# Kernel tuning notes

Hardware: AMD Instinct MI355X
Metric: run time of the kernel (lower is better)

Reference implementation:

```python
import jax, jax.numpy as jnp
import numpy as np

EMBED_DIM = 768
NUM_HEADS = 12
D_K = EMBED_DIM // NUM_HEADS


def setup_inputs() -> dict:
    key = jax.random.key(0)
    k_x, k_qkv, k_out_w, k_out_b = jax.random.split(key, 4)
    B, S = 1, 4096
    x = jax.random.normal(k_x, (B, S, EMBED_DIM), dtype=jnp.float32)
    # nn.Linear(embed_dim, 3*embed_dim, bias=False): weight [3E, E], y = x @ W^T
    scale_qkv = 1.0 / np.sqrt(EMBED_DIM)
    w_qkv = jax.random.uniform(k_qkv, (3 * EMBED_DIM, EMBED_DIM), dtype=jnp.float32,
                               minval=-scale_qkv, maxval=scale_qkv)
    w_out = jax.random.uniform(k_out_w, (EMBED_DIM, EMBED_DIM), dtype=jnp.float32,
                               minval=-scale_qkv, maxval=scale_qkv)
    b_out = jax.random.uniform(k_out_b, (EMBED_DIM,), dtype=jnp.float32,
                               minval=-scale_qkv, maxval=scale_qkv)
    return {"x": x, "w_qkv": w_qkv, "w_out": w_out, "b_out": b_out}


def reference(x, w_qkv, w_out, b_out):
    B, S, E = x.shape
    H, Dk = NUM_HEADS, D_K
    # qkv projection: [B,S,3E] -> [3,B,H,S,Dk]
    qkv = jnp.einsum('bse,fe->bsf', x, w_qkv)
    qkv = qkv.reshape(B, S, 3, H, Dk).transpose(2, 0, 3, 1, 4)
    q, k, v = qkv[0], qkv[1], qkv[2]
    # scaled dot-product attention, full [B,H,S,S] scores (naive, faithful)
    scores = jnp.einsum('bhsd,bhtd->bhst', q, k) / jnp.sqrt(jnp.float32(Dk))
    attn = jax.nn.softmax(scores, axis=-1)
    # dropout is identity in eval/deterministic baseline
    out = jnp.einsum('bhst,bhtd->bhsd', attn, v)
    out = out.transpose(0, 2, 1, 3).reshape(B, S, E)
    return jnp.einsum('bse,fe->bsf', out, w_out) + b_out
```

## Files before the change

### kernel.cpp

```cpp
#include <hip/hip_runtime.h>
#include <hip/hip_bf16.h>

constexpr int S_LEN   = 4096;
constexpr int EMB     = 768;
constexpr int NH      = 12;
constexpr int DK      = 64;
constexpr int QKV_DIM = 3 * EMB;
constexpr int NSPLIT  = 2;
constexpr int TSPLIT  = S_LEN / NSPLIT;

typedef short bf16x8 __attribute__((ext_vector_type(8)));
typedef float f32x4  __attribute__((ext_vector_type(4)));
typedef unsigned short u16;

__device__ inline u16 f2bf(float x) {
  unsigned u = __float_as_uint(x);
  unsigned r = u + 0x7fffu + ((u >> 16) & 1u);
  return (u16)(r >> 16);
}
__device__ inline float bf2f(u16 h) {
  return __uint_as_float(((unsigned)h) << 16);
}

__device__ inline void gld16(unsigned* lds, const unsigned* g) {
  __builtin_amdgcn_global_load_lds(
      (const __attribute__((address_space(1))) unsigned*)g,
      (__attribute__((address_space(3))) unsigned*)lds, 16, 0, 0);
}

#define LOG2E 1.4426950408889634f

__global__ __launch_bounds__(256) void cast_bf16(
    const float* __restrict__ src, u16* __restrict__ dst, int n8)
{
  for (int i = blockIdx.x * 256 + threadIdx.x; i < n8; i += gridDim.x * 256) {
    float4 a = reinterpret_cast<const float4*>(src)[2 * i + 0];
    float4 b = reinterpret_cast<const float4*>(src)[2 * i + 1];
    ushort4 h0, h1;
    const float* ap = reinterpret_cast<const float*>(&a);
    const float* bp = reinterpret_cast<const float*>(&b);
#pragma unroll
    for (int j = 0; j < 4; ++j) {
      reinterpret_cast<u16*>(&h0)[j] = f2bf(ap[j]);
      reinterpret_cast<u16*>(&h1)[j] = f2bf(bp[j]);
    }
    reinterpret_cast<ushort4*>(dst)[2 * i + 0] = h0;
    reinterpret_cast<ushort4*>(dst)[2 * i + 1] = h1;
  }
}

template<int MODE>
__global__ __launch_bounds__(256) void gemm_bf16_nt(
    const u16* __restrict__ A, const u16* __restrict__ B,
    const float* __restrict__ bias,
    u16* __restrict__ Cb, float* __restrict__ Cf,
    int M, int N, int K)
{
  __shared__ __align__(16) u16 sA[128 * 64];
  __shared__ __align__(16) u16 sB[128 * 64];

  const int tid  = threadIdx.x;
  const int w    = tid >> 6;
  const int l    = tid & 63;
  const int lg   = l >> 4;
  const int lr   = l & 15;
  const int wr   = w >> 1;
  const int wc   = w & 1;
  const int brow = blockIdx.x * 128;
  const int bcol = blockIdx.y * 128;

  const int srow = l >> 3;
  const int sslot = l & 7;

  f32x4 acc[4][4] = {};

  for (int k0 = 0; k0 < K; k0 += 64) {
#pragma unroll
    for (int cc = 0; cc < 4; ++cc) {
      int c = w * 4 + cc;
      int row = c * 8 + srow;
      int kswz = (sslot ^ (row & 7)) * 8;
      size_t aoff = (size_t)(brow + row) * K + k0 + kswz;
      size_t boff = (size_t)(bcol + row) * K + k0 + kswz;
      gld16((unsigned*)(sA + c * 512), (const unsigned*)(A + aoff));
      gld16((unsigned*)(sB + c * 512), (const unsigned*)(B + boff));
    }
    __syncthreads();

#pragma unroll
    for (int ks = 0; ks < 2; ++ks) {
      bf16x8 fa[4], fb[4];
#pragma unroll
      for (int i = 0; i < 4; ++i) {
        int arow = wr * 64 + i * 16 + lr;
        int brow_ = wc * 64 + i * 16 + lr;
        fa[i] = *reinterpret_cast<const bf16x8*>(
            &sA[arow * 64 + (((lg + 4 * ks) ^ (arow & 7)) << 3)]);
        fb[i] = *reinterpret_cast<const bf16x8*>(
            &sB[brow_ * 64 + (((lg + 4 * ks) ^ (brow_ & 7)) << 3)]);
      }
#pragma unroll
      for (int mi = 0; mi < 4; ++mi)
#pragma unroll
        for (int ni = 0; ni < 4; ++ni)
          acc[mi][ni] = __builtin_amdgcn_mfma_f32_16x16x32_bf16(
              fa[mi], fb[ni], acc[mi][ni], 0, 0, 0);
    }
    __syncthreads();
  }

  if (MODE == 0) {
    const float qscale = (bcol < EMB) ? 0.125f * LOG2E : 1.0f;
#pragma unroll
    for (int mi = 0; mi < 4; ++mi)
#pragma unroll
      for (int ni = 0; ni < 4; ++ni)
#pragma unroll
        for (int r = 0; r < 4; ++r) {
          size_t m = brow + wr * 64 + mi * 16 + 4 * lg + r;
          size_t n = bcol + wc * 64 + ni * 16 + lr;
          Cb[m * N + n] = f2bf(acc[mi][ni][r] * qscale);
        }
  } else {
#pragma unroll
    for (int mi = 0; mi < 4; ++mi)
#pragma unroll
      for (int ni = 0; ni < 4; ++ni)
#pragma unroll
        for (int r = 0; r < 4; ++r) {
          size_t m = brow + wr * 64 + mi * 16 + 4 * lg + r;
          size_t n = bcol + wc * 64 + ni * 16 + lr;
          Cf[m * N + n] = acc[mi][ni][r] + bias[n];
        }
  }
}

__device__ inline int key7(int row) { return (row ^ (row >> 3)) & 7; }
__device__ inline int swz16(int row, int s) {
  return row * 64 + ((s ^ key7(row)) << 3);
}
__device__ inline int swz32(int row, int p) {
  return row * 32 + ((((p >> 2) ^ key7(row)) << 2) | (p & 3));
}

__global__ __launch_bounds__(256, 3) void flash_split(
    const u16* __restrict__ qkv, float* __restrict__ Sp,
    float* __restrict__ lp)
{
  __shared__ __align__(16) u16 Ks[2][64 * 64];
  __shared__ __align__(16) u16 Vt[2][64 * 64];
  __shared__ __align__(16) u16 Ps[4][32 * 64];

  const int tid = threadIdx.x;
  const int w   = tid >> 6;
  const int l   = tid & 63;
  const int lg  = l >> 4;
  const int lr  = l & 15;

  const int bid   = blockIdx.x;
  const int sbid  = (bid & 7) * 96 + (bid >> 3);
  const int split = sbid & 1;
  const int qb    = ((sbid >> 1) & 31) * 128;
  const int h     = sbid >> 6;
  const int tbeg  = split * TSPLIT;

  unsigned* Pw = (unsigned*)Ps[w];

  const int tq  = tid >> 3;
  const int vgs = tid & 7;

  int kfO[4][2], vfO[4][2], paO[2][2], pwO[2][4], vcO[8];
#pragma unroll
  for (int tt = 0; tt < 4; ++tt)
#pragma unroll
    for (int ks = 0; ks < 2; ++ks) {
      kfO[tt][ks] = swz16(tt * 16 + lr, 4 * ks + lg);
      vfO[tt][ks] = kfO[tt][ks];
    }
#pragma unroll
  for (int qf = 0; qf < 2; ++qf) {
#pragma unroll
    for (int ks = 0; ks < 2; ++ks)
      paO[qf][ks] = swz16(qf * 16 + lr, 4 * ks + lg);
#pragma unroll
    for (int tt = 0; tt < 4; ++tt)
      pwO[qf][tt] = swz32(qf * 16 + lr, 8 * tt + 2 * lg);
  }
#pragma unroll
  for (int j = 0; j < 8; ++j)
    vcO[j] = swz32(vgs * 8 + j, tq);

  const int kt0 = tid >> 3, kg0 = tid & 7;
  const int kgo0 = kt0 * QKV_DIM + ((kg0 ^ key7(kt0)) << 3);
  const int kgo1 = (kt0 + 32) * QKV_DIM + ((kg0 ^ key7(kt0 + 32)) << 3);

  const u16* kg = qkv + EMB + h * DK + (size_t)tbeg * QKV_DIM;
  const u16* vg = qkv + 2 * EMB + h * DK +
                  ((size_t)tbeg + 2 * tq) * QKV_DIM + vgs * 8;

  bf16x8 qfr[2][2];
#pragma unroll
  for (int qf = 0; qf < 2; ++qf)
#pragma unroll
    for (int ks = 0; ks < 2; ++ks)
      qfr[qf][ks] = *reinterpret_cast<const bf16x8*>(
          qkv + (size_t)(qb + w * 32 + qf * 16 + lr) * QKV_DIM + h * DK + ks * 32 + lg * 8);

  bf16x8 ones;
#pragma unroll
  for (int i = 0; i < 8; ++i) ones[i] = (short)0x3F80;

  f32x4 acc[2][4] = {};
  f32x4 lacc[2]   = {};
  uint4 vr0, vr1;

  gld16((unsigned*)(Ks[0] + tid * 8),        (const unsigned*)(kg + kgo0));
  gld16((unsigned*)(Ks[0] + 2048 + tid * 8), (const unsigned*)(kg + kgo1));
  vr0 = *reinterpret_cast<const uint4*>(vg);
  vr1 = *reinterpret_cast<const uint4*>(vg + QKV_DIM);

  constexpr int NT = TSPLIT / 64;

#define FL_ITER(CUR, IT)                                                       \
  {                                                                            \
                              \
    {                                                                          \
      unsigned* vdst = (unsigned*)Vt[CUR];                                     \
      const unsigned* a0 = reinterpret_cast<const unsigned*>(&vr0);            \
      const unsigned* a1 = reinterpret_cast<const unsigned*>(&vr1);            \
      _Pragma("unroll")                                                        \
      for (int j = 0; j < 8; ++j) {                                            \
        unsigned sel = (j & 1) ? 0x07060302u : 0x05040100u;                    \
        vdst[vcO[j]] = __builtin_amdgcn_perm(a1[j >> 1], a0[j >> 1], sel);     \
      }                                                                        \
    }                                                                          \
    __syncthreads();                                                           \
                                         \
    if ((IT) + 1 < NT) {                                                       \
      kg += 64 * QKV_DIM;                                                      \
      vg += 64 * QKV_DIM;                                                      \
      gld16((unsigned*)(Ks[(CUR) ^ 1] + tid * 8),                              \
            (const unsigned*)(kg + kgo0));                                     \
      gld16((unsigned*)(Ks[(CUR) ^ 1] + 2048 + tid * 8),                       \
            (const unsigned*)(kg + kgo1));                                     \
      vr0 = *reinterpret_cast<const uint4*>(vg);                               \
      vr1 = *reinterpret_cast<const uint4*>(vg + QKV_DIM);                     \
    }                                                                          \
                                              \
    {                                                                          \
      bf16x8 kf[4][2];                                                         \
      _Pragma("unroll")                                                        \
      for (int tt = 0; tt < 4; ++tt) {                                         \
        kf[tt][0] = *reinterpret_cast<const bf16x8*>(&Ks[CUR][kfO[tt][0]]);    \
        kf[tt][1] = *reinterpret_cast<const bf16x8*>(&Ks[CUR][kfO[tt][1]]);    \
      }                                                                        \
      _Pragma("unroll")                                                        \
      for (int qf = 0; qf < 2; ++qf) {                                         \
        f32x4 s[4] = {};                                                       \
        __builtin_amdgcn_s_setprio(1);                                         \
        _Pragma("unroll")                                                      \
        for (int tt = 0; tt < 4; ++tt) {                                       \
          s[tt] = __builtin_amdgcn_mfma_f32_16x16x32_bf16(                     \
              kf[tt][0], qfr[qf][0], s[tt], 0, 0, 0);                          \
          s[tt] = __builtin_amdgcn_mfma_f32_16x16x32_bf16(                     \
              kf[tt][1], qfr[qf][1], s[tt], 0, 0, 0);                          \
        }                                                                      \
        __builtin_amdgcn_s_setprio(0);                                         \
        _Pragma("unroll")                                                      \
        for (int tt = 0; tt < 4; ++tt) {                                       \
          float p0 = exp2f(s[tt][0]);                                          \
          float p1 = exp2f(s[tt][1]);                                          \
          float p2 = exp2f(s[tt][2]);                                          \
          float p3 = exp2f(s[tt][3]);                                          \
          uint2 pv;                                                            \
          pv.x = __builtin_amdgcn_perm(__float_as_uint(p1),                    \
                                       __float_as_uint(p0), 0x07060302u);      \
          pv.y = __builtin_amdgcn_perm(__float_as_uint(p3),                    \
                                       __float_as_uint(p2), 0x07060302u);      \
          *reinterpret_cast<uint2*>(&Pw[pwO[qf][tt]]) = pv;                    \
        }                                                                      \
      }                                                                        \
      __builtin_amdgcn_s_setprio(1);                                           \
      _Pragma("unroll")                                                        \
      for (int ks = 0; ks < 2; ++ks) {                                         \
        bf16x8 pa[2];                                                          \
        pa[0] = *reinterpret_cast<const bf16x8*>(&Ps[w][paO[0][ks]]);          \
        pa[1] = *reinterpret_cast<const bf16x8*>(&Ps[w][paO[1][ks]]);          \
        lacc[0] = __builtin_amdgcn_mfma_f32_16x16x32_bf16(                     \
            ones, pa[0], lacc[0], 0, 0, 0);                                    \
        lacc[1] = __builtin_amdgcn_mfma_f32_16x16x32_bf16(                     \
            ones, pa[1], lacc[1], 0, 0, 0);                                    \
        _Pragma("unroll")                                                      \
        for (int dt = 0; dt < 4; ++dt) {                                       \
          bf16x8 vf = *reinterpret_cast<const bf16x8*>(&Vt[CUR][vfO[dt][ks]]); \
          acc[0][dt] = __builtin_amdgcn_mfma_f32_16x16x32_bf16(                \
              vf, pa[0], acc[0][dt], 0, 0, 0);                                 \
          acc[1][dt] = __builtin_amdgcn_mfma_f32_16x16x32_bf16(                \
              vf, pa[1], acc[1][dt], 0, 0, 0);                                 \
        }                                                                      \
      }                                                                        \
      __builtin_amdgcn_s_setprio(0);                                           \
    }                                                                          \
  }

  for (int it = 0; it < NT; it += 2) {
    FL_ITER(0, it);
    FL_ITER(1, it + 1);
  }
#undef FL_ITER

#pragma unroll
  for (int qf = 0; qf < 2; ++qf) {
    int q = qb + w * 32 + qf * 16 + lr;
    size_t base = ((size_t)split * S_LEN + q) * EMB + h * DK;
#pragma unroll
    for (int dt = 0; dt < 4; ++dt)
      *reinterpret_cast<float4*>(&Sp[base + dt * 16 + 4 * lg]) =
          *reinterpret_cast<float4*>(&acc[qf][dt]);
    if (lg == 0)
      lp[((size_t)split * NH + h) * S_LEN + q] = lacc[qf][0];
  }
}

__global__ __launch_bounds__(256) void combine_splits(
    const float* __restrict__ Sp, const float* __restrict__ lp,
    u16* __restrict__ ao)
{
  constexpr int N4 = S_LEN * EMB / 4;
  for (int i = blockIdx.x * 256 + threadIdx.x; i < N4; i += gridDim.x * 256) {
    int q = i / 192;
    int t = i - q * 192;
    int h = t >> 4;
    float la = lp[(size_t)h * S_LEN + q];
    float lb = lp[(size_t)(NH + h) * S_LEN + q];
    float inv = 1.0f / (la + lb);
    float4 s0 = reinterpret_cast<const float4*>(Sp)[i];
    float4 s1 = reinterpret_cast<const float4*>(Sp)[N4 + i];
    ushort4 o;
    o.x = f2bf((s0.x + s1.x) * inv);
    o.y = f2bf((s0.y + s1.y) * inv);
    o.z = f2bf((s0.z + s1.z) * inv);
    o.w = f2bf((s0.w + s1.w) * inv);
    reinterpret_cast<ushort4*>(ao)[i] = o;
  }
}

extern "C" void kernel_launch(void* const* d_in, const int* in_sizes, int n_in,
                              void* d_out, int out_size, void* d_ws, size_t ws_size,
                              hipStream_t stream) {
  const float* x     = (const float*)d_in[0];
  const float* w_qkv = (const float*)d_in[1];
  const float* w_out = (const float*)d_in[2];
  const float* b_out = (const float*)d_in[3];
  float* out = (float*)d_out;

  constexpr size_t NX  = (size_t)S_LEN * EMB;
  constexpr size_t NWQ = (size_t)QKV_DIM * EMB;
  constexpr size_t NWO = (size_t)EMB * EMB;
  constexpr size_t NQ  = (size_t)S_LEN * QKV_DIM;

  u16* xb    = (u16*)d_ws;
  u16* wqb   = xb + NX;
  u16* wob   = wqb + NWQ;
  u16* qkvb  = wob + NWO;
  float* Sp  = (float*)(qkvb + NQ);
  float* lp  = Sp + (size_t)NSPLIT * S_LEN * EMB;
  u16* aob   = xb;

  dim3 blk(256);

  cast_bf16<<<dim3(512), blk, 0, stream>>>(x,     xb,  (int)(NX / 8));
  cast_bf16<<<dim3(256), blk, 0, stream>>>(w_qkv, wqb, (int)(NWQ / 8));
  cast_bf16<<<dim3(128), blk, 0, stream>>>(w_out, wob, (int)(NWO / 8));

  gemm_bf16_nt<0><<<dim3(S_LEN / 128, QKV_DIM / 128), blk, 0, stream>>>(
      xb, wqb, nullptr, qkvb, nullptr, S_LEN, QKV_DIM, EMB);

  flash_split<<<dim3(768), blk, 0, stream>>>(qkvb, Sp, lp);
  combine_splits<<<dim3(1024), blk, 0, stream>>>(Sp, lp, aob);

  gemm_bf16_nt<1><<<dim3(S_LEN / 128, EMB / 128), blk, 0, stream>>>(
      aob, wob, b_out, nullptr, out, S_LEN, EMB, EMB);
}
```

Before: 144.2 us.

## Enlarge flash query tile to 256, split keys four ways, fuse cast kernels

```diff
diff --git a/kernel.cpp b/kernel.cpp
--- a/kernel.cpp
+++ b/kernel.cpp
@@ -6,7 +6,7 @@
 constexpr int NH      = 12;
 constexpr int DK      = 64;
 constexpr int QKV_DIM = 3 * EMB;
-constexpr int NSPLIT  = 2;
+constexpr int NSPLIT  = 4;
 constexpr int TSPLIT  = S_LEN / NSPLIT;
 
 typedef short bf16x8 __attribute__((ext_vector_type(8)));
@@ -28,12 +28,28 @@
       (__attribute__((address_space(3))) unsigned*)lds, 16, 0, 0);
 }
 
+__device__ inline float fast_exp2(float x) {
+#if __has_builtin(__builtin_amdgcn_exp2f)
+  return __builtin_amdgcn_exp2f(x);
+#else
+  float r;
+  asm("v_exp_f32 %0, %1" : "=v"(r) : "v"(x));
+  return r;
+#endif
+}
+
 #define LOG2E 1.4426950408889634f
 
-__global__ __launch_bounds__(256) void cast_bf16(
-    const float* __restrict__ src, u16* __restrict__ dst, int n8)
+__global__ __launch_bounds__(256) void cast_bf16_fused(
+    const float* __restrict__ s0, u16* __restrict__ d0, int n0,
+    const float* __restrict__ s1, u16* __restrict__ d1, int n1,
+    const float* __restrict__ s2, u16* __restrict__ d2, int n2)
 {
-  for (int i = blockIdx.x * 256 + threadIdx.x; i < n8; i += gridDim.x * 256) {
+  const float* src; u16* dst; int n8, b0, nb;
+  if (blockIdx.x < 512)      { src = s0; dst = d0; n8 = n0; b0 = 0;   nb = 512; }
+  else if (blockIdx.x < 768) { src = s1; dst = d1; n8 = n1; b0 = 512; nb = 256; }
+  else                       { src = s2; dst = d2; n8 = n2; b0 = 768; nb = 128; }
+  for (int i = (blockIdx.x - b0) * 256 + threadIdx.x; i < n8; i += nb * 256) {
     float4 a = reinterpret_cast<const float4*>(src)[2 * i + 0];
     float4 b = reinterpret_cast<const float4*>(src)[2 * i + 1];
     ushort4 h0, h1;
@@ -159,8 +175,8 @@
 
   const int bid   = blockIdx.x;
   const int sbid  = (bid & 7) * 96 + (bid >> 3);
-  const int split = sbid & 1;
-  const int qb    = ((sbid >> 1) & 31) * 128;
+  const int split = sbid & 3;
+  const int qb    = ((sbid >> 2) & 15) * 256;
   const int h     = sbid >> 6;
   const int tbeg  = split * TSPLIT;
 
@@ -169,22 +185,20 @@
   const int tq  = tid >> 3;
   const int vgs = tid & 7;
 
-  int kfO[4][2], vfO[4][2], paO[2][2], pwO[2][4], vcO[8];
+  int kfO[4][2], paO[2][2], pwO[2][4], vcO[8];
 #pragma unroll
   for (int tt = 0; tt < 4; ++tt)
 #pragma unroll
-    for (int ks = 0; ks < 2; ++ks) {
+    for (int ks = 0; ks < 2; ++ks)
       kfO[tt][ks] = swz16(tt * 16 + lr, 4 * ks + lg);
-      vfO[tt][ks] = kfO[tt][ks];
-    }
-#pragma unroll
-  for (int qf = 0; qf < 2; ++qf) {
+#pragma unroll
+  for (int hq = 0; hq < 2; ++hq) {
 #pragma unroll
     for (int ks = 0; ks < 2; ++ks)
-      paO[qf][ks] = swz16(qf * 16 + lr, 4 * ks + lg);
+      paO[hq][ks] = swz16(hq * 16 + lr, 4 * ks + lg);
 #pragma unroll
     for (int tt = 0; tt < 4; ++tt)
-      pwO[qf][tt] = swz32(qf * 16 + lr, 8 * tt + 2 * lg);
+      pwO[hq][tt] = swz32(hq * 16 + lr, 8 * tt + 2 * lg);
   }
 #pragma unroll
   for (int j = 0; j < 8; ++j)
@@ -198,20 +212,20 @@
   const u16* vg = qkv + 2 * EMB + h * DK +
                   ((size_t)tbeg + 2 * tq) * QKV_DIM + vgs * 8;
 
-  bf16x8 qfr[2][2];
-#pragma unroll
-  for (int qf = 0; qf < 2; ++qf)
+  bf16x8 qfr[4][2];
+#pragma unroll
+  for (int qf = 0; qf < 4; ++qf)
 #pragma unroll
     for (int ks = 0; ks < 2; ++ks)
       qfr[qf][ks] = *reinterpret_cast<const bf16x8*>(
-          qkv + (size_t)(qb + w * 32 + qf * 16 + lr) * QKV_DIM + h * DK + ks * 32 + lg * 8);
+          qkv + (size_t)(qb + w * 64 + qf * 16 + lr) * QKV_DIM + h * DK + ks * 32 + lg * 8);
 
   bf16x8 ones;
 #pragma unroll
   for (int i = 0; i < 8; ++i) ones[i] = (short)0x3F80;
 
-  f32x4 acc[2][4] = {};
-  f32x4 lacc[2]   = {};
+  f32x4 acc[4][4] = {};
+  f32x4 lacc[4]   = {};
   uint4 vr0, vr1;
 
   gld16((unsigned*)(Ks[0] + tid * 8),        (const unsigned*)(kg + kgo0));
@@ -220,6 +234,56 @@
   vr1 = *reinterpret_cast<const uint4*>(vg + QKV_DIM);
 
   constexpr int NT = TSPLIT / 64;
+
+#define QKT_PACK(QF)                                                           \
+  {                                                                            \
+    f32x4 s[4] = {};                                                           \
+    __builtin_amdgcn_s_setprio(1);                                             \
+    _Pragma("unroll")                                                          \
+    for (int tt = 0; tt < 4; ++tt) {                                           \
+      s[tt] = __builtin_amdgcn_mfma_f32_16x16x32_bf16(                         \
+          kf[tt][0], qfr[QF][0], s[tt], 0, 0, 0);                              \
+      s[tt] = __builtin_amdgcn_mfma_f32_16x16x32_bf16(                         \
+          kf[tt][1], qfr[QF][1], s[tt], 0, 0, 0);                              \
+    }                                                                          \
+    __builtin_amdgcn_s_setprio(0);                                             \
+    _Pragma("unroll")                                                          \
+    for (int tt = 0; tt < 4; ++tt) {                                           \
+      float p0 = fast_exp2(s[tt][0]);                                          \
+      float p1 = fast_exp2(s[tt][1]);                                          \
+      float p2 = fast_exp2(s[tt][2]);                                          \
+      float p3 = fast_exp2(s[tt][3]);                                          \
+      uint2 pv;                                                                \
+      pv.x = __builtin_amdgcn_perm(__float_as_uint(p1),                        \
+                                   __float_as_uint(p0), 0x07060302u);          \
+      pv.y = __builtin_amdgcn_perm(__float_as_uint(p3),                        \
+                                   __float_as_uint(p2), 0x07060302u);          \
+      *reinterpret_cast<uint2*>(&Pw[pwO[(QF) & 1][tt]]) = pv;                  \
+    }                                                                          \
+  }
+
+#define PV_HALF(HF, CUR)                                                       \
+  {                                                                            \
+    __builtin_amdgcn_s_setprio(1);                                             \
+    _Pragma("unroll")                                                          \
+    for (int ks = 0; ks < 2; ++ks) {                                           \
+      bf16x8 pa0 = *reinterpret_cast<const bf16x8*>(&Ps[w][paO[0][ks]]);       \
+      bf16x8 pa1 = *reinterpret_cast<const bf16x8*>(&Ps[w][paO[1][ks]]);       \
+      lacc[2 * (HF) + 0] = __builtin_amdgcn_mfma_f32_16x16x32_bf16(            \
+          ones, pa0, lacc[2 * (HF) + 0], 0, 0, 0);                             \
+      lacc[2 * (HF) + 1] = __builtin_amdgcn_mfma_f32_16x16x32_bf16(            \
+          ones, pa1, lacc[2 * (HF) + 1], 0, 0, 0);                             \
+      _Pragma("unroll")                                                        \
+      for (int dt = 0; dt < 4; ++dt) {                                         \
+        bf16x8 vf = *reinterpret_cast<const bf16x8*>(&Vt[CUR][kfO[dt][ks]]);   \
+        acc[2 * (HF) + 0][dt] = __builtin_amdgcn_mfma_f32_16x16x32_bf16(       \
+            vf, pa0, acc[2 * (HF) + 0][dt], 0, 0, 0);                          \
+        acc[2 * (HF) + 1][dt] = __builtin_amdgcn_mfma_f32_16x16x32_bf16(       \
+            vf, pa1, acc[2 * (HF) + 1][dt], 0, 0, 0);                          \
+      }                                                                        \
+    }                                                                          \
+    __builtin_amdgcn_s_setprio(0);                                             \
+  }
 
 #define FL_ITER(CUR, IT)                                                       \
   {                                                                            \
@@ -246,7 +310,7 @@
       vr0 = *reinterpret_cast<const uint4*>(vg);                               \
       vr1 = *reinterpret_cast<const uint4*>(vg + QKV_DIM);                     \
     }                                                                          \
-                                              \
+                   \
     {                                                                          \
       bf16x8 kf[4][2];                                                         \
       _Pragma("unroll")                                                        \
@@ -254,52 +318,12 @@
         kf[tt][0] = *reinterpret_cast<const bf16x8*>(&Ks[CUR][kfO[tt][0]]);    \
         kf[tt][1] = *reinterpret_cast<const bf16x8*>(&Ks[CUR][kfO[tt][1]]);    \
       }                                                                        \
-      _Pragma("unroll")                                                        \
-      for (int qf = 0; qf < 2; ++qf) {                                         \
-        f32x4 s[4] = {};                                                       \
-        __builtin_amdgcn_s_setprio(1);                                         \
-        _Pragma("unroll")                                                      \
-        for (int tt = 0; tt < 4; ++tt) {                                       \
-          s[tt] = __builtin_amdgcn_mfma_f32_16x16x32_bf16(                     \
-              kf[tt][0], qfr[qf][0], s[tt], 0, 0, 0);                          \
-          s[tt] = __builtin_amdgcn_mfma_f32_16x16x32_bf16(                     \
-              kf[tt][1], qfr[qf][1], s[tt], 0, 0, 0);                          \
-        }                                                                      \
-        __builtin_amdgcn_s_setprio(0);                                         \
-        _Pragma("unroll")                                                      \
-        for (int tt = 0; tt < 4; ++tt) {                                       \
-          float p0 = exp2f(s[tt][0]);                                          \
-          float p1 = exp2f(s[tt][1]);                                          \
-          float p2 = exp2f(s[tt][2]);                                          \
-          float p3 = exp2f(s[tt][3]);                                          \
-          uint2 pv;                                                            \
-          pv.x = __builtin_amdgcn_perm(__float_as_uint(p1),                    \
-                                       __float_as_uint(p0), 0x07060302u);      \
-          pv.y = __builtin_amdgcn_perm(__float_as_uint(p3),                    \
-                                       __float_as_uint(p2), 0x07060302u);      \
-          *reinterpret_cast<uint2*>(&Pw[pwO[qf][tt]]) = pv;                    \
-        }                                                                      \
-      }                                                                        \
-      __builtin_amdgcn_s_setprio(1);                                           \
-      _Pragma("unroll")                                                        \
-      for (int ks = 0; ks < 2; ++ks) {                                         \
-        bf16x8 pa[2];                                                          \
-        pa[0] = *reinterpret_cast<const bf16x8*>(&Ps[w][paO[0][ks]]);          \
-        pa[1] = *reinterpret_cast<const bf16x8*>(&Ps[w][paO[1][ks]]);          \
-        lacc[0] = __builtin_amdgcn_mfma_f32_16x16x32_bf16(                     \
-            ones, pa[0], lacc[0], 0, 0, 0);                                    \
-        lacc[1] = __builtin_amdgcn_mfma_f32_16x16x32_bf16(                     \
-            ones, pa[1], lacc[1], 0, 0, 0);                                    \
-        _Pragma("unroll")                                                      \
-        for (int dt = 0; dt < 4; ++dt) {                                       \
-          bf16x8 vf = *reinterpret_cast<const bf16x8*>(&Vt[CUR][vfO[dt][ks]]); \
-          acc[0][dt] = __builtin_amdgcn_mfma_f32_16x16x32_bf16(                \
-              vf, pa[0], acc[0][dt], 0, 0, 0);                                 \
-          acc[1][dt] = __builtin_amdgcn_mfma_f32_16x16x32_bf16(                \
-              vf, pa[1], acc[1][dt], 0, 0, 0);                                 \
-        }                                                                      \
-      }                                                                        \
-      __builtin_amdgcn_s_setprio(0);                                           \
+      QKT_PACK(0);                                                             \
+      QKT_PACK(1);                                                             \
+      PV_HALF(0, CUR);                                                         \
+      QKT_PACK(2);                                                             \
+      QKT_PACK(3);                                                             \
+      PV_HALF(1, CUR);                                                         \
     }                                                                          \
   }
 
@@ -308,10 +332,12 @@
     FL_ITER(1, it + 1);
   }
 #undef FL_ITER
-
-#pragma unroll
-  for (int qf = 0; qf < 2; ++qf) {
-    int q = qb + w * 32 + qf * 16 + lr;
+#undef PV_HALF
+#undef QKT_PACK
+
+#pragma unroll
+  for (int qf = 0; qf < 4; ++qf) {
+    int q = qb + w * 64 + qf * 16 + lr;
     size_t base = ((size_t)split * S_LEN + q) * EMB + h * DK;
 #pragma unroll
     for (int dt = 0; dt < 4; ++dt)
@@ -331,16 +357,20 @@
     int q = i / 192;
     int t = i - q * 192;
     int h = t >> 4;
-    float la = lp[(size_t)h * S_LEN + q];
-    float lb = lp[(size_t)(NH + h) * S_LEN + q];
-    float inv = 1.0f / (la + lb);
+    float lsum = 0.0f;
+#pragma unroll
+    for (int s = 0; s < NSPLIT; ++s)
+      lsum += lp[((size_t)s * NH + h) * S_LEN + q];
+    float inv = 1.0f / lsum;
     float4 s0 = reinterpret_cast<const float4*>(Sp)[i];
     float4 s1 = reinterpret_cast<const float4*>(Sp)[N4 + i];
+    float4 s2 = reinterpret_cast<const float4*>(Sp)[2 * N4 + i];
+    float4 s3 = reinterpret_cast<const float4*>(Sp)[3 * N4 + i];
     ushort4 o;
-    o.x = f2bf((s0.x + s1.x) * inv);
-    o.y = f2bf((s0.y + s1.y) * inv);
-    o.z = f2bf((s0.z + s1.z) * inv);
-    o.w = f2bf((s0.w + s1.w) * inv);
+    o.x = f2bf((s0.x + s1.x + s2.x + s3.x) * inv);
+    o.y = f2bf((s0.y + s1.y + s2.y + s3.y) * inv);
+    o.z = f2bf((s0.z + s1.z + s2.z + s3.z) * inv);
+    o.w = f2bf((s0.w + s1.w + s2.w + s3.w) * inv);
     reinterpret_cast<ushort4*>(ao)[i] = o;
   }
 }
@@ -369,9 +399,8 @@
 
   dim3 blk(256);
 
-  cast_bf16<<<dim3(512), blk, 0, stream>>>(x,     xb,  (int)(NX / 8));
-  cast_bf16<<<dim3(256), blk, 0, stream>>>(w_qkv, wqb, (int)(NWQ / 8));
-  cast_bf16<<<dim3(128), blk, 0, stream>>>(w_out, wob, (int)(NWO / 8));
+  cast_bf16_fused<<<dim3(896), blk, 0, stream>>>(
+      x, xb, (int)(NX / 8), w_qkv, wqb, (int)(NWQ / 8), w_out, wob, (int)(NWO / 8));
 
   gemm_bf16_nt<0><<<dim3(S_LEN / 128, QKV_DIM / 128), blk, 0, stream>>>(
       xb, wqb, nullptr, qkvb, nullptr, S_LEN, QKV_DIM, EMB);
```

After: 338.2 us. 2.35x slower.

## Use four KV splits with 256-row Q tiles, fast exp2, fused casts

Applied to the files above, without the earlier changes.

```diff
diff --git a/kernel.cpp b/kernel.cpp
--- a/kernel.cpp
+++ b/kernel.cpp
@@ -6,7 +6,7 @@
 constexpr int NH      = 12;
 constexpr int DK      = 64;
 constexpr int QKV_DIM = 3 * EMB;
-constexpr int NSPLIT  = 2;
+constexpr int NSPLIT  = 4;
 constexpr int TSPLIT  = S_LEN / NSPLIT;
 
 typedef short bf16x8 __attribute__((ext_vector_type(8)));
@@ -28,12 +28,28 @@
       (__attribute__((address_space(3))) unsigned*)lds, 16, 0, 0);
 }
 
+__device__ inline float fast_exp2(float x) {
+#if __has_builtin(__builtin_amdgcn_exp2f)
+  return __builtin_amdgcn_exp2f(x);
+#else
+  float r;
+  asm("v_exp_f32 %0, %1" : "=v"(r) : "v"(x));
+  return r;
+#endif
+}
+
 #define LOG2E 1.4426950408889634f
 
-__global__ __launch_bounds__(256) void cast_bf16(
-    const float* __restrict__ src, u16* __restrict__ dst, int n8)
+__global__ __launch_bounds__(256) void cast_bf16_fused(
+    const float* __restrict__ s0, u16* __restrict__ d0, int n0,
+    const float* __restrict__ s1, u16* __restrict__ d1, int n1,
+    const float* __restrict__ s2, u16* __restrict__ d2, int n2)
 {
-  for (int i = blockIdx.x * 256 + threadIdx.x; i < n8; i += gridDim.x * 256) {
+  const float* src; u16* dst; int n8, b0, nb;
+  if (blockIdx.x < 512)      { src = s0; dst = d0; n8 = n0; b0 = 0;   nb = 512; }
+  else if (blockIdx.x < 768) { src = s1; dst = d1; n8 = n1; b0 = 512; nb = 256; }
+  else                       { src = s2; dst = d2; n8 = n2; b0 = 768; nb = 128; }
+  for (int i = (blockIdx.x - b0) * 256 + threadIdx.x; i < n8; i += nb * 256) {
     float4 a = reinterpret_cast<const float4*>(src)[2 * i + 0];
     float4 b = reinterpret_cast<const float4*>(src)[2 * i + 1];
     ushort4 h0, h1;
@@ -143,13 +159,13 @@
   return row * 32 + ((((p >> 2) ^ key7(row)) << 2) | (p & 3));
 }
 
-__global__ __launch_bounds__(256, 3) void flash_split(
+__global__ __launch_bounds__(256) void flash_split(
     const u16* __restrict__ qkv, float* __restrict__ Sp,
     float* __restrict__ lp)
 {
   __shared__ __align__(16) u16 Ks[2][64 * 64];
   __shared__ __align__(16) u16 Vt[2][64 * 64];
-  __shared__ __align__(16) u16 Ps[4][32 * 64];
+  __shared__ __align__(16) u16 Ps[4][64 * 64];
 
   const int tid = threadIdx.x;
   const int w   = tid >> 6;
@@ -159,8 +175,8 @@
 
   const int bid   = blockIdx.x;
   const int sbid  = (bid & 7) * 96 + (bid >> 3);
-  const int split = sbid & 1;
-  const int qb    = ((sbid >> 1) & 31) * 128;
+  const int split = sbid & 3;
+  const int qb    = ((sbid >> 2) & 15) * 256;
   const int h     = sbid >> 6;
   const int tbeg  = split * TSPLIT;
 
@@ -169,16 +185,14 @@
   const int tq  = tid >> 3;
   const int vgs = tid & 7;
 
-  int kfO[4][2], vfO[4][2], paO[2][2], pwO[2][4], vcO[8];
+  int kfO[4][2], paO[4][2], pwO[4][4], vcO[8];
 #pragma unroll
   for (int tt = 0; tt < 4; ++tt)
 #pragma unroll
-    for (int ks = 0; ks < 2; ++ks) {
+    for (int ks = 0; ks < 2; ++ks)
       kfO[tt][ks] = swz16(tt * 16 + lr, 4 * ks + lg);
-      vfO[tt][ks] = kfO[tt][ks];
-    }
-#pragma unroll
-  for (int qf = 0; qf < 2; ++qf) {
+#pragma unroll
+  for (int qf = 0; qf < 4; ++qf) {
 #pragma unroll
     for (int ks = 0; ks < 2; ++ks)
       paO[qf][ks] = swz16(qf * 16 + lr, 4 * ks + lg);
@@ -198,20 +212,20 @@
   const u16* vg = qkv + 2 * EMB + h * DK +
                   ((size_t)tbeg + 2 * tq) * QKV_DIM + vgs * 8;
 
-  bf16x8 qfr[2][2];
-#pragma unroll
-  for (int qf = 0; qf < 2; ++qf)
+  bf16x8 qfr[4][2];
+#pragma unroll
+  for (int qf = 0; qf < 4; ++qf)
 #pragma unroll
     for (int ks = 0; ks < 2; ++ks)
       qfr[qf][ks] = *reinterpret_cast<const bf16x8*>(
-          qkv + (size_t)(qb + w * 32 + qf * 16 + lr) * QKV_DIM + h * DK + ks * 32 + lg * 8);
+          qkv + (size_t)(qb + w * 64 + qf * 16 + lr) * QKV_DIM + h * DK + ks * 32 + lg * 8);
 
   bf16x8 ones;
 #pragma unroll
   for (int i = 0; i < 8; ++i) ones[i] = (short)0x3F80;
 
-  f32x4 acc[2][4] = {};
-  f32x4 lacc[2]   = {};
+  f32x4 acc[4][4] = {};
+  f32x4 lacc[4]   = {};
   uint4 vr0, vr1;
 
   gld16((unsigned*)(Ks[0] + tid * 8),        (const unsigned*)(kg + kgo0));
@@ -255,7 +269,7 @@
         kf[tt][1] = *reinterpret_cast<const bf16x8*>(&Ks[CUR][kfO[tt][1]]);    \
       }                                                                        \
       _Pragma("unroll")                                                        \
-      for (int qf = 0; qf < 2; ++qf) {                                         \
+      for (int qf = 0; qf < 4; ++qf) {                                         \
         f32x4 s[4] = {};                                                       \
         __builtin_amdgcn_s_setprio(1);                                         \
         _Pragma("unroll")                                                      \
@@ -268,10 +282,10 @@
         __builtin_amdgcn_s_setprio(0);                                         \
         _Pragma("unroll")                                                      \
         for (int tt = 0; tt < 4; ++tt) {                                       \
-          float p0 = exp2f(s[tt][0]);                                          \
-          float p1 = exp2f(s[tt][1]);                                          \
-          float p2 = exp2f(s[tt][2]);                                          \
-          float p3 = exp2f(s[tt][3]);                                          \
+          float p0 = fast_exp2(s[tt][0]);                                      \
+          float p1 = fast_exp2(s[tt][1]);                                      \
+          float p2 = fast_exp2(s[tt][2]);                                      \
+          float p3 = fast_exp2(s[tt][3]);                                      \
           uint2 pv;                                                            \
           pv.x = __builtin_amdgcn_perm(__float_as_uint(p1),                    \
                                        __float_as_uint(p0), 0x07060302u);      \
@@ -283,20 +297,20 @@
       __builtin_amdgcn_s_setprio(1);                                           \
       _Pragma("unroll")                                                        \
       for (int ks = 0; ks < 2; ++ks) {                                         \
-        bf16x8 pa[2];                                                          \
-        pa[0] = *reinterpret_cast<const bf16x8*>(&Ps[w][paO[0][ks]]);          \
-        pa[1] = *reinterpret_cast<const bf16x8*>(&Ps[w][paO[1][ks]]);          \
-        lacc[0] = __builtin_amdgcn_mfma_f32_16x16x32_bf16(                     \
-            ones, pa[0], lacc[0], 0, 0, 0);                                    \
-        lacc[1] = __builtin_amdgcn_mfma_f32_16x16x32_bf16(                     \
-            ones, pa[1], lacc[1], 0, 0, 0);                                    \
+        bf16x8 pa[4];                                                          \
+        _Pragma("unroll")                                                      \
+        for (int qf = 0; qf < 4; ++qf) {                                       \
+          pa[qf] = *reinterpret_cast<const bf16x8*>(&Ps[w][paO[qf][ks]]);      \
+          lacc[qf] = __builtin_amdgcn_mfma_f32_16x16x32_bf16(                  \
+              ones, pa[qf], lacc[qf], 0, 0, 0);                                \
+        }                                                                      \
         _Pragma("unroll")                                                      \
         for (int dt = 0; dt < 4; ++dt) {                                       \
-          bf16x8 vf = *reinterpret_cast<const bf16x8*>(&Vt[CUR][vfO[dt][ks]]); \
-          acc[0][dt] = __builtin_amdgcn_mfma_f32_16x16x32_bf16(                \
-              vf, pa[0], acc[0][dt], 0, 0, 0);                                 \
-          acc[1][dt] = __builtin_amdgcn_mfma_f32_16x16x32_bf16(                \
-              vf, pa[1], acc[1][dt], 0, 0, 0);                                 \
+          bf16x8 vf = *reinterpret_cast<const bf16x8*>(&Vt[CUR][kfO[dt][ks]]); \
+          _Pragma("unroll")                                                    \
+          for (int qf = 0; qf < 4; ++qf)                                       \
+            acc[qf][dt] = __builtin_amdgcn_mfma_f32_16x16x32_bf16(             \
+                vf, pa[qf], acc[qf][dt], 0, 0, 0);                             \
         }                                                                      \
       }                                                                        \
       __builtin_amdgcn_s_setprio(0);                                           \
@@ -310,8 +324,8 @@
 #undef FL_ITER
 
 #pragma unroll
-  for (int qf = 0; qf < 2; ++qf) {
-    int q = qb + w * 32 + qf * 16 + lr;
+  for (int qf = 0; qf < 4; ++qf) {
+    int q = qb + w * 64 + qf * 16 + lr;
     size_t base = ((size_t)split * S_LEN + q) * EMB + h * DK;
 #pragma unroll
     for (int dt = 0; dt < 4; ++dt)
@@ -331,16 +345,20 @@
     int q = i / 192;
     int t = i - q * 192;
     int h = t >> 4;
-    float la = lp[(size_t)h * S_LEN + q];
-    float lb = lp[(size_t)(NH + h) * S_LEN + q];
-    float inv = 1.0f / (la + lb);
+    float lsum = 0.0f;
+#pragma unroll
+    for (int s = 0; s < NSPLIT; ++s)
+      lsum += lp[((size_t)s * NH + h) * S_LEN + q];
+    float inv = 1.0f / lsum;
     float4 s0 = reinterpret_cast<const float4*>(Sp)[i];
     float4 s1 = reinterpret_cast<const float4*>(Sp)[N4 + i];
+    float4 s2 = reinterpret_cast<const float4*>(Sp)[2 * N4 + i];
+    float4 s3 = reinterpret_cast<const float4*>(Sp)[3 * N4 + i];
     ushort4 o;
-    o.x = f2bf((s0.x + s1.x) * inv);
-    o.y = f2bf((s0.y + s1.y) * inv);
-    o.z = f2bf((s0.z + s1.z) * inv);
-    o.w = f2bf((s0.w + s1.w) * inv);
+    o.x = f2bf((s0.x + s1.x + s2.x + s3.x) * inv);
+    o.y = f2bf((s0.y + s1.y + s2.y + s3.y) * inv);
+    o.z = f2bf((s0.z + s1.z + s2.z + s3.z) * inv);
+    o.w = f2bf((s0.w + s1.w + s2.w + s3.w) * inv);
     reinterpret_cast<ushort4*>(ao)[i] = o;
   }
 }
@@ -369,9 +387,8 @@
 
   dim3 blk(256);
 
-  cast_bf16<<<dim3(512), blk, 0, stream>>>(x,     xb,  (int)(NX / 8));
-  cast_bf16<<<dim3(256), blk, 0, stream>>>(w_qkv, wqb, (int)(NWQ / 8));
-  cast_bf16<<<dim3(128), blk, 0, stream>>>(w_out, wob, (int)(NWO / 8));
+  cast_bf16_fused<<<dim3(896), blk, 0, stream>>>(
+      x, xb, (int)(NX / 8), w_qkv, wqb, (int)(NWQ / 8), w_out, wob, (int)(NWO / 8));
 
   gemm_bf16_nt<0><<<dim3(S_LEN / 128, QKV_DIM / 128), blk, 0, stream>>>(
       xb, wqb, nullptr, qkvb, nullptr, S_LEN, QKV_DIM, EMB);
```

Result: slower. 163.0 us (+13.0%).
